# Kernel optimization log

Measured on AMD Instinct MI355X. Metric: run time of the kernel, lower is better.

Reference implementation:

```python
import jax, jax.numpy as jnp
import numpy as np

N = 50000      # num nodes
E = 1600000    # num edges (avg degree 32)
D = 256        # in_feats
H = 256        # hidden_feats
EPS = 1e-5


def setup_inputs() -> dict:
    key = jax.random.key(0)
    ks = jax.random.split(key, 9)
    x = jax.random.normal(ks[0], (N, D), jnp.float32)
    src = jax.random.randint(ks[1], (E,), 0, N)
    dst = jax.random.randint(ks[2], (E,), 0, N)
    W1 = jax.random.normal(ks[3], (D, H), jnp.float32) / np.sqrt(D).astype(np.float32)
    b1 = jnp.zeros((H,), jnp.float32)
    W2 = jax.random.normal(ks[4], (H, H), jnp.float32) / np.sqrt(H).astype(np.float32)
    b2 = jnp.zeros((H,), jnp.float32)
    gamma = jnp.ones((H,), jnp.float32)
    beta = jnp.zeros((H,), jnp.float32)
    return {"x": x, "W1": W1, "b1": b1, "W2": W2, "b2": b2,
            "gamma": gamma, "beta": beta, "src": src, "dst": dst}


def _gcn_conv(x, src, dst, W, b):
    # DGL GraphConv with norm='both': h = D_in^{-1/2} A (D_out^{-1/2} x) W + b
    ones = jnp.ones((src.shape[0],), x.dtype)
    deg_out = jnp.maximum(jax.ops.segment_sum(ones, src, num_segments=N), 1.0)
    deg_in = jnp.maximum(jax.ops.segment_sum(ones, dst, num_segments=N), 1.0)
    h = x * (deg_out ** -0.5)[:, None]
    # project first (in >= out) to keep message width small, same math
    h = h @ W
    m = jax.ops.segment_sum(h[src], dst, num_segments=N)  # [N, H]
    return m * (deg_in ** -0.5)[:, None] + b


def _layer_norm(h, gamma, beta):
    mu = jnp.mean(h, axis=-1, keepdims=True)
    var = jnp.mean(jnp.square(h - mu), axis=-1, keepdims=True)
    return (h - mu) * jax.lax.rsqrt(var + EPS) * gamma + beta


def reference(x, W1, b1, W2, b2, gamma, beta, src, dst):
    h = _gcn_conv(x, src, dst, W1, b1)
    h = jax.nn.relu(h)
    # dropout is identity in eval mode
    h = _gcn_conv(h, src, dst, W2, b2)
    h = _layer_norm(h, gamma, beta)
    return h
```

## Files before the change

### kernel.cpp

```cpp
#include <hip/hip_runtime.h>

#define NN 50000
#define EE 1600000
#define HD 256
#define MPAD 50048
#define LN_EPS 1e-5f

#define NB 256
#define BR 196
#define NBLK 128
#define CH 12500
#define SL 16
#define SSH 12
#define FB 3136
#define FBP 3328
#define CF 13

typedef unsigned short ushort_t;
typedef unsigned int uint_t;

using frag_ab = __attribute__((ext_vector_type(8))) short;
using frag_cd = __attribute__((ext_vector_type(4))) float;

__device__ __forceinline__ ushort_t f2bf(float f) {
    uint_t u = __float_as_uint(f);
    uint_t r = (u + 0x7FFFu + ((u >> 16) & 1u)) >> 16;
    return (ushort_t)r;
}
__device__ __forceinline__ float blo(uint_t u) { return __uint_as_float(u << 16); }
__device__ __forceinline__ float bhi(uint_t u) { return __uint_as_float(u & 0xFFFF0000u); }

__global__ __launch_bounds__(256) void radix_count(
    const int* __restrict__ src, const int* __restrict__ dst,
    int* __restrict__ cntD, int* __restrict__ cntS)
{
    __shared__ int hD[NB], hS[NB];
    int t = threadIdx.x, blk = blockIdx.x;
    hD[t] = 0; hS[t] = 0;
    __syncthreads();
    for (int i = t; i < CH; i += 256) {
        int e = blk * CH + i;
        atomicAdd(&hD[dst[e] / BR], 1);
        atomicAdd(&hS[src[e] / BR], 1);
    }
    __syncthreads();
    cntD[t * NBLK + blk] = hD[t];
    cntS[t * NBLK + blk] = hS[t];
}

__global__ __launch_bounds__(256) void radix_scan(
    const int* __restrict__ cntD, int* __restrict__ scanD, int* __restrict__ bbD,
    const int* __restrict__ cntS, int* __restrict__ scanS, int* __restrict__ bbS)
{
    const int* cnt = (blockIdx.x == 0) ? cntD : cntS;
    int* scn       = (blockIdx.x == 0) ? scanD : scanS;
    int* bb        = (blockIdx.x == 0) ? bbD : bbS;
    int t = threadIdx.x, lane = t & 63, wv = t >> 6;
    int base = t * NBLK;
    int s = 0;
    for (int j = 0; j < NBLK; j++) s += cnt[base + j];
    int sc = s;
    #pragma unroll
    for (int off = 1; off < 64; off <<= 1) {
        int nv = __shfl_up(sc, off);
        if (lane >= off) sc += nv;
    }
    __shared__ int wp[4];
    if (lane == 63) wp[wv] = sc;
    __syncthreads();
    int wb = 0;
    for (int w = 0; w < wv; w++) wb += wp[w];
    int run = wb + sc - s;
    bb[t] = run;
    for (int j = 0; j < NBLK; j++) { scn[base + j] = run; run += cnt[base + j]; }
    if (t == 255) bb[256] = run;
}

__global__ __launch_bounds__(256) void radix_scatter(
    const int* __restrict__ src, const int* __restrict__ dst,
    const int* __restrict__ scanD, const int* __restrict__ scanS,
    uint2* __restrict__ dpart, int* __restrict__ spart)
{
    __shared__ int curD[NB], curS[NB];
    int t = threadIdx.x, blk = blockIdx.x;
    curD[t] = scanD[t * NBLK + blk];
    curS[t] = scanS[t * NBLK + blk];
    __syncthreads();
    for (int i = t; i < CH; i += 256) {
        int e = blk * CH + i;
        int sv = src[e], dv = dst[e];
        int pd = atomicAdd(&curD[dv / BR], 1);
        dpart[pd] = make_uint2((uint_t)sv, (uint_t)dv);
        int ps = atomicAdd(&curS[sv / BR], 1);
        spart[ps] = sv;
    }
}

__global__ __launch_bounds__(256) void fine_dst(
    const uint2* __restrict__ dpart, const int* __restrict__ bbD,
    int* __restrict__ rp16, int* __restrict__ csr_src)
{
    __shared__ int hist[FBP];
    __shared__ int cur[FBP];
    __shared__ int wp[4];
    int t = threadIdx.x, lane = t & 63, wv = t >> 6;
    int b = blockIdx.x;
    int bb = bbD[b];
    int cnt = bbD[b + 1] - bb;
    int node0 = b * BR;
    #pragma unroll
    for (int j = 0; j < CF; j++) hist[t * CF + j] = 0;
    __syncthreads();
    for (int i = t; i < cnt; i += 256) {
        uint2 p = dpart[bb + i];
        int bin = ((int)p.y - node0) * SL + ((int)p.x >> SSH);
        atomicAdd(&hist[bin], 1);
    }
    __syncthreads();
    int vals[CF];
    int s = 0;
    #pragma unroll
    for (int j = 0; j < CF; j++) { vals[j] = hist[t * CF + j]; s += vals[j]; }
    int sc = s;
    #pragma unroll
    for (int off = 1; off < 64; off <<= 1) {
        int nv = __shfl_up(sc, off);
        if (lane >= off) sc += nv;
    }
    if (lane == 63) wp[wv] = sc;
    __syncthreads();
    int wb = 0;
    for (int w = 0; w < wv; w++) wb += wp[w];
    int run = wb + sc - s;
    #pragma unroll
    for (int j = 0; j < CF; j++) {
        int bin = t * CF + j;
        cur[bin] = run;
        if (bin < FB) rp16[b * FB + bin] = bb + run;
        run += vals[j];
    }
    __syncthreads();
    for (int i = t; i < cnt; i += 256) {
        uint2 p = dpart[bb + i];
        int bin = ((int)p.y - node0) * SL + ((int)p.x >> SSH);
        int pos = bb + atomicAdd(&cur[bin], 1);
        csr_src[pos] = (int)p.x;
    }
}

__global__ __launch_bounds__(256) void fine_src(
    const int* __restrict__ spart, const int* __restrict__ bbS,
    int* __restrict__ deg_out)
{
    __shared__ int hist[NB];
    int t = threadIdx.x, b = blockIdx.x;
    hist[t] = 0;
    __syncthreads();
    int bb = bbS[b];
    int cnt = bbS[b + 1] - bb;
    int node0 = b * BR;
    for (int i = t; i < cnt; i += 256) atomicAdd(&hist[spart[bb + i] - node0], 1);
    __syncthreads();
    if (t < BR) deg_out[node0 + t] = hist[t];
}

__global__ void wconv(const float* __restrict__ W, ushort_t* __restrict__ Wt) {
    int g = blockIdx.x * 256 + threadIdx.x;
    int k = g >> 8, n = g & 255;
    Wt[n * 256 + k] = f2bf(W[g]);
}

__device__ __forceinline__ int swz(int r, int kElem) {
    return ((r * 64 + kElem) * 2) ^ ((r & 7) << 4);
}

template <int A_BF16>
__global__ __launch_bounds__(256) void gemm_mfma(
    const void* __restrict__ Aptr, const ushort_t* __restrict__ Wt,
    const int* __restrict__ deg, ushort_t* __restrict__ Y)
{
    __shared__ __align__(16) ushort_t As[8192];
    __shared__ __align__(16) ushort_t Bs[8192];
    __shared__ float sS[128];

    int t = threadIdx.x;
    int lane = t & 63, wid = t >> 6;
    int wm = wid >> 1, wn = wid & 1;
    int row0 = blockIdx.x * 128;
    int col0 = blockIdx.y * 128;

    if (t < 128) {
        int row = row0 + t;
        int dg = (row < NN) ? deg[row] : 1;
        sS[t] = rsqrtf((float)(dg > 1 ? dg : 1));
    }

    frag_cd acc[4][4];
    #pragma unroll
    for (int m = 0; m < 4; m++)
        #pragma unroll
        for (int n = 0; n < 4; n++) acc[m][n] = (frag_cd)(0.f);

    const float*    Af = (const float*)Aptr;
    const ushort_t* Ab = (const ushort_t*)Aptr;

    for (int k0 = 0; k0 < HD; k0 += 64) {
        __syncthreads();
        #pragma unroll
        for (int i = 0; i < 8; i++) {
            int flat = i * 256 + t;
            int r = flat >> 4;
            int k4 = (flat & 15) * 4;
            int row = row0 + r;
            ushort4 u;
            if constexpr (!A_BF16) {
                float4 v = make_float4(0.f, 0.f, 0.f, 0.f);
                if (row < NN) v = *(const float4*)&Af[(size_t)row * 256 + k0 + k4];
                u.x = f2bf(v.x); u.y = f2bf(v.y); u.z = f2bf(v.z); u.w = f2bf(v.w);
            } else {
                if (row < NN) u = *(const ushort4*)&Ab[(size_t)row * 256 + k0 + k4];
                else u = make_ushort4(0, 0, 0, 0);
            }
            *(ushort4*)((char*)As + swz(r, k4)) = u;
        }
        #pragma unroll
        for (int i = 0; i < 8; i++) {
            int flat = i * 256 + t;
            int nn = flat >> 4;
            int k4 = (flat & 15) * 4;
            ushort4 u = *(const ushort4*)&Wt[(size_t)(col0 + nn) * 256 + k0 + k4];
            *(ushort4*)((char*)Bs + swz(nn, k4)) = u;
        }
        __syncthreads();
        #pragma unroll
        for (int s = 0; s < 2; s++) {
            int kb = s * 32 + ((lane >> 4) * 8);
            frag_ab af[4], bfr[4];
            #pragma unroll
            for (int m = 0; m < 4; m++) {
                int r = wm * 64 + m * 16 + (lane & 15);
                af[m] = *(const frag_ab*)((const char*)As + swz(r, kb));
            }
            #pragma unroll
            for (int n = 0; n < 4; n++) {
                int c = wn * 64 + n * 16 + (lane & 15);
                bfr[n] = *(const frag_ab*)((const char*)Bs + swz(c, kb));
            }
            #pragma unroll
            for (int m = 0; m < 4; m++)
                #pragma unroll
                for (int n = 0; n < 4; n++)
                    acc[m][n] = __builtin_amdgcn_mfma_f32_16x16x32_bf16(
                        af[m], bfr[n], acc[m][n], 0, 0, 0);
        }
    }

    #pragma unroll
    for (int m = 0; m < 4; m++) {
        int rl = wm * 64 + m * 16 + ((lane >> 4) * 4);
        #pragma unroll
        for (int j = 0; j < 4; j++) {
            float sc = sS[rl + j];
            size_t grow = (size_t)(row0 + rl + j);
            #pragma unroll
            for (int n = 0; n < 4; n++) {
                int gcol = col0 + wn * 64 + n * 16 + (lane & 15);
                Y[grow * 256 + gcol] = f2bf(acc[m][n][j] * sc);
            }
        }
    }
}

template <int MODE>
__global__ __launch_bounds__(256) void aggregate_kernel(
    const ushort_t* __restrict__ msg, const int* __restrict__ rp16,
    const int* __restrict__ csr_src,
    const float* __restrict__ bias, const float* __restrict__ gamma,
    const float* __restrict__ beta, void* __restrict__ outp)
{
    int wv = threadIdx.x >> 6, lane = threadIdx.x & 63;
    int n = blockIdx.x * 4 + wv;
    if (n >= NN) return;
    int start = rp16[n * SL];
    int end   = rp16[n * SL + SL];
    int cnt = end - start;
    int i = start;
    float a0 = 0.f, a1 = 0.f, a2 = 0.f, a3 = 0.f;
    const uint2* base = (const uint2*)msg;

    for (; i + 8 <= end; i += 8) {
        int ss[8];
        #pragma unroll
        for (int u = 0; u < 8; u++) ss[u] = csr_src[i + u];
        uint2 vv[8];
        #pragma unroll
        for (int u = 0; u < 8; u++) vv[u] = base[(size_t)ss[u] * 64 + lane];
        #pragma unroll
        for (int u = 0; u < 8; u++) {
            a0 += blo(vv[u].x); a1 += bhi(vv[u].x);
            a2 += blo(vv[u].y); a3 += bhi(vv[u].y);
        }
    }
    for (; i < end; i++) {
        int s = csr_src[i];
        uint2 v = base[(size_t)s * 64 + lane];
        a0 += blo(v.x); a1 += bhi(v.x); a2 += blo(v.y); a3 += bhi(v.y);
    }

    float scl = rsqrtf((float)(cnt > 1 ? cnt : 1));
    float4 b = ((const float4*)bias)[lane];
    float r0 = a0 * scl + b.x;
    float r1 = a1 * scl + b.y;
    float r2 = a2 * scl + b.z;
    float r3 = a3 * scl + b.w;

    if (MODE == 0) {
        r0 = fmaxf(r0, 0.f); r1 = fmaxf(r1, 0.f);
        r2 = fmaxf(r2, 0.f); r3 = fmaxf(r3, 0.f);
        uint2 o;
        o.x = (uint_t)f2bf(r0) | ((uint_t)f2bf(r1) << 16);
        o.y = (uint_t)f2bf(r2) | ((uint_t)f2bf(r3) << 16);
        ((uint2*)outp)[(size_t)n * 64 + lane] = o;
    } else {
        float s1 = r0 + r1 + r2 + r3;
        #pragma unroll
        for (int off = 1; off < 64; off <<= 1) s1 += __shfl_xor(s1, off);
        float mu = s1 * (1.f / 256.f);
        float d0 = r0 - mu, d1 = r1 - mu, d2 = r2 - mu, d3 = r3 - mu;
        float s2 = d0 * d0 + d1 * d1 + d2 * d2 + d3 * d3;
        #pragma unroll
        for (int off = 1; off < 64; off <<= 1) s2 += __shfl_xor(s2, off);
        float rs = rsqrtf(s2 * (1.f / 256.f) + LN_EPS);
        float4 g  = ((const float4*)gamma)[lane];
        float4 be = ((const float4*)beta)[lane];
        float4 o;
        o.x = d0 * rs * g.x + be.x;
        o.y = d1 * rs * g.y + be.y;
        o.z = d2 * rs * g.z + be.z;
        o.w = d3 * rs * g.w + be.w;
        ((float4*)outp)[(size_t)n * 64 + lane] = o;
    }
}

extern "C" void kernel_launch(void* const* d_in, const int* in_sizes, int n_in,
                              void* d_out, int out_size, void* d_ws, size_t ws_size,
                              hipStream_t stream)
{
    const float* x     = (const float*)d_in[0];
    const float* W1    = (const float*)d_in[1];
    const float* b1    = (const float*)d_in[2];
    const float* W2    = (const float*)d_in[3];
    const float* b2    = (const float*)d_in[4];
    const float* gamma = (const float*)d_in[5];
    const float* beta  = (const float*)d_in[6];
    const int*   src   = (const int*)d_in[7];
    const int*   dst   = (const int*)d_in[8];
    float* out = (float*)d_out;

    uint2*    dpart  = (uint2*)d_ws;
    ushort_t* msg    = (ushort_t*)(dpart + EE);
    int*      csr    = (int*)(msg + (size_t)MPAD * 256);
    int*      spart  = csr + EE;
    int*      rp16   = spart + EE;
    int*      cntD   = rp16 + NB * FB + 16;
    int*      cntS   = cntD + NB * NBLK;
    int*      scanD  = cntS + NB * NBLK;
    int*      scanS  = scanD + NB * NBLK;
    int*      bbD    = scanS + NB * NBLK;
    int*      bbS    = bbD + 320;
    int*      degout = bbS + 320;
    ushort_t* Wt1    = (ushort_t*)(degout + NB * BR);
    ushort_t* Wt2    = Wt1 + 65536;

    ushort_t* h = (ushort_t*)d_out;

    radix_count  <<<NBLK, 256, 0, stream>>>(src, dst, cntD, cntS);
    radix_scan   <<<2, 256, 0, stream>>>(cntD, scanD, bbD, cntS, scanS, bbS);
    radix_scatter<<<NBLK, 256, 0, stream>>>(src, dst, scanD, scanS, dpart, spart);
    fine_dst     <<<NB, 256, 0, stream>>>(dpart, bbD, rp16, csr);
    fine_src     <<<NB, 256, 0, stream>>>(spart, bbS, degout);

    wconv<<<256, 256, 0, stream>>>(W1, Wt1);
    wconv<<<256, 256, 0, stream>>>(W2, Wt2);

    dim3 gg(MPAD / 128, 2);
    gemm_mfma<0><<<gg, 256, 0, stream>>>(x, Wt1, degout, msg);
    aggregate_kernel<0><<<(NN + 3) / 4, 256, 0, stream>>>(msg, rp16, csr,
                                                          b1, nullptr, nullptr, h);
    gemm_mfma<1><<<gg, 256, 0, stream>>>(h, Wt2, degout, msg);
    aggregate_kernel<1><<<(NN + 3) / 4, 256, 0, stream>>>(msg, rp16, csr,
                                                          b2, gamma, beta, out);
}
```

Measured before the change: 487.9 us.

## Phase aggregation by source-slice so concurrent warps gather from a shared source range

Each warp now owns 13 consecutive destination nodes and walks the 16 source slices in order. For each slice it gathers the matching edges of every owned node, so warps running at the same time touch a narrower window of message rows and get better L2 reuse. The grid becomes a fixed 1024 blocks with a launch-bounds occupancy hint, and each warp keeps 52 accumulators in registers. A sentinel row-pointer write is added so the per-slice end index exists for the last node. The cost is higher register pressure, shorter inner loops with less memory-level parallelism, and fewer warps in flight.

```diff
diff --git a/kernel.cpp b/kernel.cpp
--- a/kernel.cpp
+++ b/kernel.cpp
@@ -16,6 +16,9 @@
 #define FBP 3328
 #define CF 13
 
+#define AGG_BLOCKS 1024
+#define NPW 13
+
 typedef unsigned short ushort_t;
 typedef unsigned int uint_t;
 
@@ -139,6 +142,7 @@
         if (bin < FB) rp16[b * FB + bin] = bb + run;
         run += vals[j];
     }
+    if (b == NB - 1 && t == 0) rp16[NB * FB] = bbD[NB];
     __syncthreads();
     for (int i = t; i < cnt; i += 256) {
         uint2 p = dpart[bb + i];
@@ -272,73 +276,97 @@
 }
 
 template <int MODE>
-__global__ __launch_bounds__(256) void aggregate_kernel(
+__global__ __launch_bounds__(256, 4) void aggregate_phased(
     const ushort_t* __restrict__ msg, const int* __restrict__ rp16,
     const int* __restrict__ csr_src,
     const float* __restrict__ bias, const float* __restrict__ gamma,
     const float* __restrict__ beta, void* __restrict__ outp)
 {
-    int wv = threadIdx.x >> 6, lane = threadIdx.x & 63;
-    int n = blockIdx.x * 4 + wv;
-    if (n >= NN) return;
-    int start = rp16[n * SL];
-    int end   = rp16[n * SL + SL];
-    int cnt = end - start;
-    int i = start;
-    float a0 = 0.f, a1 = 0.f, a2 = 0.f, a3 = 0.f;
+    int lane = threadIdx.x & 63;
+    int gw = blockIdx.x * 4 + (threadIdx.x >> 6);
+    int n0 = gw * NPW;
+    if (n0 >= NB * BR) return;
+
+    float a[NPW][4];
+    #pragma unroll
+    for (int j = 0; j < NPW; j++) { a[j][0] = a[j][1] = a[j][2] = a[j][3] = 0.f; }
     const uint2* base = (const uint2*)msg;
 
-    for (; i + 8 <= end; i += 8) {
-        int ss[8];
-        #pragma unroll
-        for (int u = 0; u < 8; u++) ss[u] = csr_src[i + u];
-        uint2 vv[8];
-        #pragma unroll
-        for (int u = 0; u < 8; u++) vv[u] = base[(size_t)ss[u] * 64 + lane];
-        #pragma unroll
-        for (int u = 0; u < 8; u++) {
-            a0 += blo(vv[u].x); a1 += bhi(vv[u].x);
-            a2 += blo(vv[u].y); a3 += bhi(vv[u].y);
-        }
-    }
-    for (; i < end; i++) {
-        int s = csr_src[i];
-        uint2 v = base[(size_t)s * 64 + lane];
-        a0 += blo(v.x); a1 += bhi(v.x); a2 += blo(v.y); a3 += bhi(v.y);
-    }
-
-    float scl = rsqrtf((float)(cnt > 1 ? cnt : 1));
-    float4 b = ((const float4*)bias)[lane];
-    float r0 = a0 * scl + b.x;
-    float r1 = a1 * scl + b.y;
-    float r2 = a2 * scl + b.z;
-    float r3 = a3 * scl + b.w;
-
-    if (MODE == 0) {
-        r0 = fmaxf(r0, 0.f); r1 = fmaxf(r1, 0.f);
-        r2 = fmaxf(r2, 0.f); r3 = fmaxf(r3, 0.f);
-        uint2 o;
-        o.x = (uint_t)f2bf(r0) | ((uint_t)f2bf(r1) << 16);
-        o.y = (uint_t)f2bf(r2) | ((uint_t)f2bf(r3) << 16);
-        ((uint2*)outp)[(size_t)n * 64 + lane] = o;
-    } else {
-        float s1 = r0 + r1 + r2 + r3;
-        #pragma unroll
-        for (int off = 1; off < 64; off <<= 1) s1 += __shfl_xor(s1, off);
-        float mu = s1 * (1.f / 256.f);
-        float d0 = r0 - mu, d1 = r1 - mu, d2 = r2 - mu, d3 = r3 - mu;
-        float s2 = d0 * d0 + d1 * d1 + d2 * d2 + d3 * d3;
-        #pragma unroll
-        for (int off = 1; off < 64; off <<= 1) s2 += __shfl_xor(s2, off);
-        float rs = rsqrtf(s2 * (1.f / 256.f) + LN_EPS);
-        float4 g  = ((const float4*)gamma)[lane];
-        float4 be = ((const float4*)beta)[lane];
-        float4 o;
-        o.x = d0 * rs * g.x + be.x;
-        o.y = d1 * rs * g.y + be.y;
-        o.z = d2 * rs * g.z + be.z;
-        o.w = d3 * rs * g.w + be.w;
-        ((float4*)outp)[(size_t)n * 64 + lane] = o;
+    for (int s = 0; s < SL; s++) {
+        #pragma unroll
+        for (int j = 0; j < NPW; j++) {
+            int n = n0 + j;
+            if (n >= NB * BR) continue;
+            int i  = rp16[n * SL + s];
+            int en = rp16[n * SL + s + 1];
+            for (; i + 4 <= en; i += 4) {
+                int i0 = csr_src[i], i1 = csr_src[i + 1];
+                int i2 = csr_src[i + 2], i3 = csr_src[i + 3];
+                uint2 v0 = base[(size_t)i0 * 64 + lane];
+                uint2 v1 = base[(size_t)i1 * 64 + lane];
+                uint2 v2 = base[(size_t)i2 * 64 + lane];
+                uint2 v3 = base[(size_t)i3 * 64 + lane];
+                a[j][0] += blo(v0.x) + blo(v1.x) + blo(v2.x) + blo(v3.x);
+                a[j][1] += bhi(v0.x) + bhi(v1.x) + bhi(v2.x) + bhi(v3.x);
+                a[j][2] += blo(v0.y) + blo(v1.y) + blo(v2.y) + blo(v3.y);
+                a[j][3] += bhi(v0.y) + bhi(v1.y) + bhi(v2.y) + bhi(v3.y);
+            }
+            if (i + 2 <= en) {
+                int i0 = csr_src[i], i1 = csr_src[i + 1];
+                uint2 v0 = base[(size_t)i0 * 64 + lane];
+                uint2 v1 = base[(size_t)i1 * 64 + lane];
+                a[j][0] += blo(v0.x) + blo(v1.x);
+                a[j][1] += bhi(v0.x) + bhi(v1.x);
+                a[j][2] += blo(v0.y) + blo(v1.y);
+                a[j][3] += bhi(v0.y) + bhi(v1.y);
+                i += 2;
+            }
+            if (i < en) {
+                int i0 = csr_src[i];
+                uint2 v0 = base[(size_t)i0 * 64 + lane];
+                a[j][0] += blo(v0.x); a[j][1] += bhi(v0.x);
+                a[j][2] += blo(v0.y); a[j][3] += bhi(v0.y);
+            }
+        }
+    }
+
+    float4 b  = ((const float4*)bias)[lane];
+    #pragma unroll
+    for (int j = 0; j < NPW; j++) {
+        int n = n0 + j;
+        if (n >= NN) continue;
+        int cnt = rp16[n * SL + SL] - rp16[n * SL];
+        float scl = rsqrtf((float)(cnt > 1 ? cnt : 1));
+        float r0 = a[j][0] * scl + b.x;
+        float r1 = a[j][1] * scl + b.y;
+        float r2 = a[j][2] * scl + b.z;
+        float r3 = a[j][3] * scl + b.w;
+        if (MODE == 0) {
+            r0 = fmaxf(r0, 0.f); r1 = fmaxf(r1, 0.f);
+            r2 = fmaxf(r2, 0.f); r3 = fmaxf(r3, 0.f);
+            uint2 o;
+            o.x = (uint_t)f2bf(r0) | ((uint_t)f2bf(r1) << 16);
+            o.y = (uint_t)f2bf(r2) | ((uint_t)f2bf(r3) << 16);
+            ((uint2*)outp)[(size_t)n * 64 + lane] = o;
+        } else {
+            float s1 = r0 + r1 + r2 + r3;
+            #pragma unroll
+            for (int off = 1; off < 64; off <<= 1) s1 += __shfl_xor(s1, off);
+            float mu = s1 * (1.f / 256.f);
+            float d0 = r0 - mu, d1 = r1 - mu, d2 = r2 - mu, d3 = r3 - mu;
+            float s2 = d0 * d0 + d1 * d1 + d2 * d2 + d3 * d3;
+            #pragma unroll
+            for (int off = 1; off < 64; off <<= 1) s2 += __shfl_xor(s2, off);
+            float rs = rsqrtf(s2 * (1.f / 256.f) + LN_EPS);
+            float4 g  = ((const float4*)gamma)[lane];
+            float4 be = ((const float4*)beta)[lane];
+            float4 o;
+            o.x = d0 * rs * g.x + be.x;
+            o.y = d1 * rs * g.y + be.y;
+            o.z = d2 * rs * g.z + be.z;
+            o.w = d3 * rs * g.w + be.w;
+            ((float4*)outp)[(size_t)n * 64 + lane] = o;
+        }
     }
 }
 
@@ -385,9 +413,9 @@
 
     dim3 gg(MPAD / 128, 2);
     gemm_mfma<0><<<gg, 256, 0, stream>>>(x, Wt1, degout, msg);
-    aggregate_kernel<0><<<(NN + 3) / 4, 256, 0, stream>>>(msg, rp16, csr,
-                                                          b1, nullptr, nullptr, h);
+    aggregate_phased<0><<<AGG_BLOCKS, 256, 0, stream>>>(msg, rp16, csr,
+                                                        b1, nullptr, nullptr, h);
     gemm_mfma<1><<<gg, 256, 0, stream>>>(h, Wt2, degout, msg);
-    aggregate_kernel<1><<<(NN + 3) / 4, 256, 0, stream>>>(msg, rp16, csr,
-                                                          b2, gamma, beta, out);
-}
+    aggregate_phased<1><<<AGG_BLOCKS, 256, 0, stream>>>(msg, rp16, csr,
+                                                        b2, gamma, beta, out);
+}
```

Measured after the change: 703.8 us. +44.3%, slower.
